# Performance work log

Measured on AMD Instinct MI355X. Metric: run time of the kernel, lower is better.

## Reference

```python
import jax, jax.numpy as jnp
import numpy as np

B, S, H, NH, NL, G, D, A, T = 32, 512, 512, 8, 6, 8, 256, 18, 1024
HD = H // NH


def setup_inputs() -> dict:
    key = jax.random.key(0)
    ks = jax.random.split(key, 32)
    def n(k, shape, s=0.02):
        return jax.random.normal(k, shape, jnp.float32) * s
    return {
        'game_indices': jax.random.randint(ks[0], (B,), 0, G),
        'states': jax.random.normal(ks[1], (B, S, D), jnp.float32),
        'actions': jax.random.randint(ks[2], (B, S), 0, A),
        'returns_to_go': jax.random.normal(ks[3], (B, S), jnp.float32),
        'timesteps': jax.random.randint(ks[4], (B, S), 0, T),
        'attention_mask': jnp.ones((B, S), jnp.int32),
        'game_emb': n(ks[5], (G, H)),
        'obs_W': n(ks[6], (G, D, H)),
        'obs_b': n(ks[7], (G, H)),
        'obs_ln_g': jnp.ones((G, H), jnp.float32),
        'obs_ln_b': jnp.zeros((G, H), jnp.float32),
        'act_emb': n(ks[8], (G, A, H)),
        'ret_W': n(ks[9], (H,)),
        'ret_b': n(ks[10], (H,)),
        'time_emb': n(ks[11], (T, H)),
        'Wqkv': n(ks[12], (NL, 3 * H, H)),
        'bqkv': n(ks[13], (NL, 3 * H)),
        'Wo': n(ks[14], (NL, H, H)),
        'bo': n(ks[15], (NL, H)),
        'ln1_g': jnp.ones((NL, H), jnp.float32),
        'ln1_b': jnp.zeros((NL, H), jnp.float32),
        'W1': n(ks[16], (NL, 4 * H, H)),
        'b1': n(ks[17], (NL, 4 * H)),
        'W2': n(ks[18], (NL, H, 4 * H)),
        'b2': n(ks[19], (NL, H)),
        'ln2_g': jnp.ones((NL, H), jnp.float32),
        'ln2_b': jnp.zeros((NL, H), jnp.float32),
        'sh_W': n(ks[20], (G, H, D)),
        'sh_b': n(ks[21], (G, D)),
        'ah_W': n(ks[22], (G, H, A)),
        'ah_b': n(ks[23], (G, A)),
        'rh_W': n(ks[24], (H, 1)),
        'rh_b': n(ks[25], (1,)),
    }


def _ln(x, g, b, eps=1e-5):
    m = jnp.mean(x, -1, keepdims=True)
    v = jnp.mean((x - m) ** 2, -1, keepdims=True)
    return (x - m) / jnp.sqrt(v + eps) * g + b


def reference(game_indices, states, actions, returns_to_go, timesteps, attention_mask,
              game_emb, obs_W, obs_b, obs_ln_g, obs_ln_b, act_emb, ret_W, ret_b, time_emb,
              Wqkv, bqkv, Wo, bo, ln1_g, ln1_b, W1, b1, W2, b2, ln2_g, ln2_b,
              sh_W, sh_b, ah_W, ah_b, rh_W, rh_b):
    gi = game_indices
    g_emb = game_emb[gi][:, None, :]  # [B,1,H]
    # per-game routed observation embedding: Linear -> LayerNorm -> ReLU (grouped GEMM by game)
    se = jnp.einsum('bsd,bdh->bsh', states, obs_W[gi]) + obs_b[gi][:, None, :]
    se = jax.nn.relu(_ln(se, obs_ln_g[gi][:, None, :], obs_ln_b[gi][:, None, :]))
    # per-game routed action embedding table lookup
    ae = act_emb[gi[:, None], actions]  # [B,S,H]
    re = returns_to_go[..., None] * ret_W + ret_b  # Linear(1,H)
    te = time_emb[timesteps]
    x = se + ae + re + te + g_emb
    # key padding mask (src_key_padding_mask: True where attention_mask==0)
    bias = jnp.where((attention_mask == 0)[:, None, None, :], -1e9, 0.0)  # [B,1,1,S]
    scale = 1.0 / jnp.sqrt(jnp.asarray(HD, jnp.float32))
    for l in range(NL):  # post-norm TransformerEncoderLayer, relu, dropout=0 (eval)
        qkv = jnp.einsum('bsh,oh->bso', x, Wqkv[l]) + bqkv[l]
        q, k, v = jnp.split(qkv, 3, axis=-1)
        q = q.reshape(B, S, NH, HD).transpose(0, 2, 1, 3)
        k = k.reshape(B, S, NH, HD).transpose(0, 2, 1, 3)
        v = v.reshape(B, S, NH, HD).transpose(0, 2, 1, 3)
        scores = jnp.einsum('bhqd,bhkd->bhqk', q, k) * scale + bias
        attn = jnp.einsum('bhqk,bhkd->bhqd', jax.nn.softmax(scores, -1), v)
        attn = attn.transpose(0, 2, 1, 3).reshape(B, S, H)
        attn = jnp.einsum('bsh,oh->bso', attn, Wo[l]) + bo[l]
        x = _ln(x + attn, ln1_g[l], ln1_b[l])
        ff = jax.nn.relu(jnp.einsum('bsh,fh->bsf', x, W1[l]) + b1[l])
        ff = jnp.einsum('bsf,hf->bsh', ff, W2[l]) + b2[l]
        x = _ln(x + ff, ln2_g[l], ln2_b[l])
    # per-game routed prediction heads
    state_preds = jnp.einsum('bsh,bho->bso', x, sh_W[gi]) + sh_b[gi][:, None, :]
    action_preds = jnp.einsum('bsh,bho->bso', x, ah_W[gi]) + ah_b[gi][:, None, :]
    return_preds = x @ rh_W + rh_b
    return (state_preds, action_preds, return_preds)
```

## Files before the change

kernel.cpp:

```cpp
#include <hip/hip_runtime.h>

typedef __bf16 bf16x4 __attribute__((ext_vector_type(4)));
typedef __bf16 bf16x8 __attribute__((ext_vector_type(8)));
typedef float f32x4 __attribute__((ext_vector_type(4)));
typedef int int4v __attribute__((ext_vector_type(4)));

#define C1SM  0.18033688011112042592f

typedef const __attribute__((address_space(1))) void gvoid_t;
typedef __attribute__((address_space(3))) void lvoid_t;


__global__ void cvt_f32_bf16(const float* __restrict__ src, __bf16* __restrict__ dst, int n4)
{
    int i = blockIdx.x * blockDim.x + threadIdx.x;
    if (i >= n4) return;
    f32x4 v = *reinterpret_cast<const f32x4*>(src + (size_t)i * 4);
    bf16x4 o;
    #pragma unroll
    for (int k = 0; k < 4; ++k) o[k] = (__bf16)v[k];
    *reinterpret_cast<bf16x4*>(dst + (size_t)i * 4) = o;
}

__global__ void transpose_cvt(const float* __restrict__ src, __bf16* __restrict__ dst, int R, int C)
{
    int m = blockIdx.y;
    int n = R * C;
    int i = blockIdx.x * 256 + threadIdx.x;
    if (i >= n) return;
    int c = i / R, r = i - c * R;
    dst[(size_t)m * n + i] = (__bf16)src[(size_t)m * n + (size_t)r * C + c];
}

__global__ void transpose_f32(const float* __restrict__ src, float* __restrict__ dst, int R, int C)
{
    int m = blockIdx.y;
    int n = R * C;
    int i = blockIdx.x * 256 + threadIdx.x;
    if (i >= n) return;
    int c = i / R, r = i - c * R;
    dst[(size_t)m * n + i] = src[(size_t)m * n + (size_t)r * C + c];
}

__global__ __launch_bounds__(256, 4)
void gemm_bt(const __bf16* __restrict__ A, size_t strideA,
             const __bf16* __restrict__ B, size_t strideB,
             const float* __restrict__ bias, int strideBias,
             float* Cf, __bf16* Cb, size_t strideC,
             const int* __restrict__ gidx,
             int K, int ldc, int relu, __bf16* __restrict__ vt)
{
    __shared__ __align__(16) char smem[32768];
    __bf16* lCb = (__bf16*)smem;
    float*  lCf = (float*)smem;

    const int z = blockIdx.z;
    const int g = gidx ? gidx[z] : 0;
    const __bf16* Ab = A + (size_t)z * strideA;
    const __bf16* Bb = B + (size_t)g * strideB;

    const int nx = gridDim.x;
    const int nwg = nx * gridDim.y;
    int orig = blockIdx.y * nx + blockIdx.x;
    int wg = ((nwg & 7) == 0) ? ((orig & 7) * (nwg >> 3) + (orig >> 3)) : orig;
    const int bm = (wg / nx) * 128, bn = (wg % nx) * 128;

    const int t = threadIdx.x;
    const int w = t >> 6, lane = t & 63;
    const int wr = (w >> 1) * 64, wc = (w & 1) * 64;
    const int l16 = lane & 15, lk = lane >> 4;

    const int srow = lane >> 2;
    const int schunk = (lane & 3) ^ (srow & 3);
    const int ca = (lk ^ (l16 & 3)) * 8;

    f32x4 acc[4][4] = {};

    auto stage = [&](int buf, int kt) {
        __bf16* la = (__bf16*)(smem + buf * 16384);
        __bf16* lb = la + 4096;
        #pragma unroll
        for (int jj = 0; jj < 2; ++jj) {
            const __bf16* ga = Ab + (size_t)(bm + w * 32 + jj * 16 + srow) * K + kt + schunk * 8;
            __builtin_amdgcn_global_load_lds((gvoid_t*)ga, (lvoid_t*)&la[(w * 32 + jj * 16) * 32], 16, 0, 0);
            const __bf16* gb = Bb + (size_t)(bn + w * 32 + jj * 16 + srow) * K + kt + schunk * 8;
            __builtin_amdgcn_global_load_lds((gvoid_t*)gb, (lvoid_t*)&lb[(w * 32 + jj * 16) * 32], 16, 0, 0);
        }
    };

    stage(0, 0);
    __syncthreads();
    int cur = 0;
    for (int kt = 0; kt < K; kt += 32) {
        if (kt + 32 < K) stage(cur ^ 1, kt + 32);
        __bf16* la = (__bf16*)(smem + cur * 16384);
        __bf16* lb = la + 4096;
        bf16x8 af[4], bfr[4];
        #pragma unroll
        for (int i = 0; i < 4; ++i) {
            af[i]  = *reinterpret_cast<const bf16x8*>(&la[(wr + i * 16 + l16) * 32 + ca]);
            bfr[i] = *reinterpret_cast<const bf16x8*>(&lb[(wc + i * 16 + l16) * 32 + ca]);
        }
        #pragma unroll
        for (int mi = 0; mi < 4; ++mi)
            #pragma unroll
            for (int ni = 0; ni < 4; ++ni)
                acc[mi][ni] = __builtin_amdgcn_mfma_f32_16x16x32_bf16(af[mi], bfr[ni], acc[mi][ni], 0, 0, 0);
        __syncthreads();
        cur ^= 1;
    }

    const float* biasb = bias ? bias + (size_t)g * strideBias : nullptr;

    if (vt && bn >= 1024) {
        const int bb = bm >> 9;
        const int s0 = (bm & 511) + wr + lk * 4;
        #pragma unroll
        for (int ni = 0; ni < 4; ++ni) {
            int c = bn + wc + ni * 16 + l16;
            float bv = biasb ? biasb[c] : 0.f;
            int hh = (c - 1024) >> 6, d = c & 63;
            __bf16* vrow = vt + ((size_t)(bb * 8 + hh) * 64 + d) * 512;
            #pragma unroll
            for (int mi = 0; mi < 4; ++mi) {
                bf16x4 o;
                #pragma unroll
                for (int j = 0; j < 4; ++j) o[j] = (__bf16)(acc[mi][ni][j] + bv);
                *reinterpret_cast<bf16x4*>(vrow + s0 + mi * 16) = o;
            }
        }
        return;
    }

    if (Cb) {
        #pragma unroll
        for (int ni = 0; ni < 4; ++ni) {
            int col = wc + ni * 16 + l16;
            float bv = biasb ? biasb[bn + col] : 0.f;
            #pragma unroll
            for (int mi = 0; mi < 4; ++mi)
                #pragma unroll
                for (int j = 0; j < 4; ++j) {
                    float v = acc[mi][ni][j] + bv;
                    if (relu) v = fmaxf(v, 0.f);
                    lCb[(wr + mi * 16 + lk * 4 + j) * 128 + col] = (__bf16)v;
                }
        }
        __syncthreads();
        #pragma unroll
        for (int it = 0; it < 8; ++it) {
            int off = it * 2048 + t * 8;
            int rl = off >> 7, col = off & 127;
            *reinterpret_cast<int4v*>(Cb + (size_t)z * strideC + (size_t)(bm + rl) * ldc + bn + col) =
                *reinterpret_cast<const int4v*>(&lCb[off]);
        }
    } else {
        #pragma unroll
        for (int p = 0; p < 2; ++p) {
            if (p) __syncthreads();
            if (wr == p * 64) {
                #pragma unroll
                for (int ni = 0; ni < 4; ++ni) {
                    int col = wc + ni * 16 + l16;
                    float bv = biasb ? biasb[bn + col] : 0.f;
                    #pragma unroll
                    for (int mi = 0; mi < 4; ++mi)
                        #pragma unroll
                        for (int j = 0; j < 4; ++j) {
                            float v = acc[mi][ni][j] + bv;
                            if (relu) v = fmaxf(v, 0.f);
                            lCf[(mi * 16 + lk * 4 + j) * 128 + col] = v;
                        }
                }
            }
            __syncthreads();
            #pragma unroll
            for (int it = 0; it < 8; ++it) {
                int off = it * 1024 + t * 4;
                int rl = off >> 7, col = off & 127;
                *reinterpret_cast<f32x4*>(Cf + (size_t)z * strideC + (size_t)(bm + p * 64 + rl) * ldc + bn + col) =
                    *reinterpret_cast<const f32x4*>(&lCf[off]);
            }
        }
    }
}

__global__ __launch_bounds__(256, 6)
void attn_fwd(const __bf16* __restrict__ qkv, const __bf16* __restrict__ vt,
              const int* __restrict__ mask, __bf16* __restrict__ out)
{
    __shared__ __bf16 lK[2][64 * 64];
    __shared__ __bf16 lP[4][16 * 32];
    __shared__ float lM2[512];

    const int bh = blockIdx.x;
    const int b = bh >> 3, h = bh & 7;
    const int q0 = blockIdx.y * 64;
    const int t = threadIdx.x, w = t >> 6, lane = t & 63;
    const int l16 = lane & 15, lk = lane >> 4;

    const __bf16* qbase = qkv + (size_t)b * 512 * 1536 + h * 64;
    const __bf16* kbase = qbase + 512;
    const __bf16* vtb = vt + (size_t)(b * 8 + h) * 64 * 512;

    bf16x8 qfr[2];
    {
        int row = q0 + w * 16 + l16;
        #pragma unroll
        for (int kc = 0; kc < 2; ++kc)
            qfr[kc] = *reinterpret_cast<const bf16x8*>(qbase + (size_t)row * 1536 + (kc * 4 + lk) * 8);
    }

    {
        int i0 = t * 2;
        lM2[i0]     = (mask[b * 512 + i0] == 0)     ? -2e9f : 0.f;
        lM2[i0 + 1] = (mask[b * 512 + i0 + 1] == 0) ? -2e9f : 0.f;
    }

    auto stageK = [&](int buf, int kt) {
        #pragma unroll
        for (int r = 0; r < 2; ++r) {
            int c = r * 256 + w * 64 + lane;
            int row = c >> 3, ch = c & 7;
            const __bf16* ga = kbase + (size_t)(kt + row) * 1536 + ((ch ^ (row & 7)) * 8);
            __builtin_amdgcn_global_load_lds((gvoid_t*)ga,
                (lvoid_t*)(&lK[buf][0] + (r * 256 + w * 64) * 8), 16, 0, 0);
        }
    };

    float m_run = -1e30f, l_run = 0.f;
    f32x4 oacc[4] = {};
    const int xsw = ((l16 >> 1) & 3) << 1;

    stageK(0, 0);
    __syncthreads();

    int cur = 0;
    for (int kt = 0; kt < 512; kt += 64) {
        if (kt + 64 < 512) stageK(cur ^ 1, kt + 64);
        const __bf16* lKc = &lK[cur][0];

        f32x4 sacc[4] = {};
        #pragma unroll
        for (int ni = 0; ni < 4; ++ni) {
            int krow = ni * 16 + l16;
            #pragma unroll
            for (int kc = 0; kc < 2; ++kc) {
                bf16x8 kf = *reinterpret_cast<const bf16x8*>(&lKc[krow * 64 + (((kc * 4 + lk) ^ (krow & 7)) * 8)]);
                sacc[ni] = __builtin_amdgcn_mfma_f32_16x16x32_bf16(kf, qfr[kc], sacc[ni], 0, 0, 0);
            }
        }

        f32x4 mx4 = {-3e38f, -3e38f, -3e38f, -3e38f};
        #pragma unroll
        for (int ni = 0; ni < 4; ++ni) {
            f32x4 mkv = *reinterpret_cast<const f32x4*>(&lM2[kt + ni * 16 + lk * 4]);
            f32x4 sv;
            #pragma unroll
            for (int j = 0; j < 4; ++j) {
                sv[j] = fmaf(sacc[ni][j], C1SM, mkv[j]);
                mx4[j] = fmaxf(mx4[j], sv[j]);
            }
            sacc[ni] = sv;
        }
        float mx = fmaxf(fmaxf(mx4[0], mx4[1]), fmaxf(mx4[2], mx4[3]));
        mx = fmaxf(mx, __shfl_xor(mx, 16));
        mx = fmaxf(mx, __shfl_xor(mx, 32));
        bool need = mx > m_run + 11.54f;
        if (__any((int)need)) {
            float mn = fmaxf(m_run, mx);
            float alpha = exp2f(m_run - mn);
            m_run = mn;
            l_run *= alpha;
            #pragma unroll
            for (int j = 0; j < 4; ++j) {
                float aj = __shfl(alpha, lk * 4 + j);
                #pragma unroll
                for (int dn = 0; dn < 4; ++dn) oacc[dn][j] *= aj;
            }
        }
        f32x4 ps4 = {0.f, 0.f, 0.f, 0.f};
        #pragma unroll
        for (int ni = 0; ni < 4; ++ni)
            #pragma unroll
            for (int j = 0; j < 4; ++j) {
                float p = exp2f(sacc[ni][j] - m_run);
                sacc[ni][j] = p;
                ps4[j] += p;
            }
        l_run += (ps4[0] + ps4[1]) + (ps4[2] + ps4[3]);

        __bf16* lp = &lP[w][0];
        #pragma unroll
        for (int kc = 0; kc < 2; ++kc) {
            #pragma unroll
            for (int n2 = 0; n2 < 2; ++n2) {
                bf16x4 o;
                #pragma unroll
                for (int j = 0; j < 4; ++j) o[j] = (__bf16)sacc[kc * 2 + n2][j];
                *reinterpret_cast<bf16x4*>(&lp[l16 * 32 + ((n2 * 4 + lk) ^ xsw) * 4]) = o;
            }
            bf16x8 pf = *reinterpret_cast<const bf16x8*>(&lp[l16 * 32 + (lk ^ (xsw >> 1)) * 8]);
            #pragma unroll
            for (int dn = 0; dn < 4; ++dn) {
                bf16x8 vf = *reinterpret_cast<const bf16x8*>(vtb + (size_t)(dn * 16 + l16) * 512 + kt + kc * 32 + lk * 8);
                oacc[dn] = __builtin_amdgcn_mfma_f32_16x16x32_bf16(pf, vf, oacc[dn], 0, 0, 0);
            }
        }
        __syncthreads();
        cur ^= 1;
    }

    float s = l_run;
    s += __shfl_xor(s, 16);
    s += __shfl_xor(s, 32);
    float linv = 1.f / s;
    #pragma unroll
    for (int j = 0; j < 4; ++j) {
        float lj = __shfl(linv, lk * 4 + j);
        #pragma unroll
        for (int dn = 0; dn < 4; ++dn) {
            int row = q0 + w * 16 + lk * 4 + j;
            int col = h * 64 + dn * 16 + l16;
            out[(size_t)(b * 512 + row) * 512 + col] = (__bf16)(oacc[dn][j] * lj);
        }
    }
}


__device__ __forceinline__ float wsum64(float v)
{
    #pragma unroll
    for (int d = 32; d >= 1; d >>= 1) v += __shfl_xor(v, d);
    return v;
}

__global__ __launch_bounds__(256)
void ln_fuse(const float* resid, const __bf16* __restrict__ proj,
             const float* __restrict__ gamma, const float* __restrict__ beta,
             float* xfo, __bf16* __restrict__ xbo)
{
    int tok = blockIdx.x * 4 + (threadIdx.x >> 6);
    int lane = threadIdx.x & 63;
    size_t base = (size_t)tok * 512 + lane * 8;
    float y[8];
    {
        f32x4 a0 = *reinterpret_cast<const f32x4*>(resid + base);
        f32x4 a1 = *reinterpret_cast<const f32x4*>(resid + base + 4);
        bf16x8 pv = *reinterpret_cast<const bf16x8*>(proj + base);
        #pragma unroll
        for (int i = 0; i < 4; ++i) { y[i] = a0[i] + (float)pv[i]; y[4 + i] = a1[i] + (float)pv[4 + i]; }
    }
    float s = 0.f;
    #pragma unroll
    for (int i = 0; i < 8; ++i) s += y[i];
    float mean = wsum64(s) * (1.f / 512.f);
    float v = 0.f;
    #pragma unroll
    for (int i = 0; i < 8; ++i) { float d = y[i] - mean; v += d * d; }
    float rstd = rsqrtf(wsum64(v) * (1.f / 512.f) + 1e-5f);
    int hh = lane * 8;
    f32x4 g0 = *reinterpret_cast<const f32x4*>(gamma + hh);
    f32x4 g1 = *reinterpret_cast<const f32x4*>(gamma + hh + 4);
    f32x4 b0 = *reinterpret_cast<const f32x4*>(beta + hh);
    f32x4 b1 = *reinterpret_cast<const f32x4*>(beta + hh + 4);
    f32x4 o0, o1;
    bf16x8 ob;
    #pragma unroll
    for (int i = 0; i < 4; ++i) {
        float t0 = (y[i] - mean) * rstd * g0[i] + b0[i];
        float t1 = (y[4 + i] - mean) * rstd * g1[i] + b1[i];
        o0[i] = t0; o1[i] = t1;
        ob[i] = (__bf16)t0; ob[4 + i] = (__bf16)t1;
    }
    *reinterpret_cast<f32x4*>(xfo + base) = o0;
    *reinterpret_cast<f32x4*>(xfo + base + 4) = o1;
    *reinterpret_cast<bf16x8*>(xbo + base) = ob;
}

__global__ __launch_bounds__(256)
void embed_fin(const __bf16* __restrict__ seraw, const int* __restrict__ gi,
               const int* __restrict__ actions, const float* __restrict__ rtg,
               const int* __restrict__ ts,
               const float* __restrict__ olg, const float* __restrict__ olb,
               const float* __restrict__ act_emb, const float* __restrict__ retW,
               const float* __restrict__ retb, const float* __restrict__ time_emb,
               const float* __restrict__ game_emb,
               float* __restrict__ xfo, __bf16* __restrict__ xbo)
{
    int tok = blockIdx.x * 4 + (threadIdx.x >> 6);
    int lane = threadIdx.x & 63;
    int b = tok >> 9;
    int g = gi[b];
    int a = actions[tok];
    int tt = ts[tok];
    float rv = rtg[tok];
    size_t base = (size_t)tok * 512 + lane * 8;
    int hh = lane * 8;

    float y[8];
    {
        bf16x8 a0 = *reinterpret_cast<const bf16x8*>(seraw + base);
        #pragma unroll
        for (int i = 0; i < 8; ++i) y[i] = (float)a0[i];
    }
    float s = 0.f;
    #pragma unroll
    for (int i = 0; i < 8; ++i) s += y[i];
    float mean = wsum64(s) * (1.f / 512.f);
    float v = 0.f;
    #pragma unroll
    for (int i = 0; i < 8; ++i) { float d = y[i] - mean; v += d * d; }
    float rstd = rsqrtf(wsum64(v) * (1.f / 512.f) + 1e-5f);

    const float* gp = olg + (size_t)g * 512 + hh;
    const float* bp = olb + (size_t)g * 512 + hh;
    const float* ap = act_emb + ((size_t)g * 18 + a) * 512 + hh;
    const float* tp = time_emb + (size_t)tt * 512 + hh;
    const float* ep = game_emb + (size_t)g * 512 + hh;
    const float* rwp = retW + hh;
    const float* rbp = retb + hh;

    f32x4 o0, o1;
    bf16x8 ob;
    #pragma unroll
    for (int half = 0; half < 2; ++half) {
        f32x4 gv = *reinterpret_cast<const f32x4*>(gp + half * 4);
        f32x4 bv = *reinterpret_cast<const f32x4*>(bp + half * 4);
        f32x4 av = *reinterpret_cast<const f32x4*>(ap + half * 4);
        f32x4 tv = *reinterpret_cast<const f32x4*>(tp + half * 4);
        f32x4 ev = *reinterpret_cast<const f32x4*>(ep + half * 4);
        f32x4 rw = *reinterpret_cast<const f32x4*>(rwp + half * 4);
        f32x4 rb = *reinterpret_cast<const f32x4*>(rbp + half * 4);
        #pragma unroll
        for (int i = 0; i < 4; ++i) {
            float n = (y[half * 4 + i] - mean) * rstd * gv[i] + bv[i];
            n = fmaxf(n, 0.f);
            float o = n + av[i] + rv * rw[i] + rb[i] + tv[i] + ev[i];
            if (half == 0) o0[i] = o; else o1[i] = o;
            ob[half * 4 + i] = (__bf16)o;
        }
    }
    *reinterpret_cast<f32x4*>(xfo + base) = o0;
    *reinterpret_cast<f32x4*>(xfo + base + 4) = o1;
    *reinterpret_cast<bf16x8*>(xbo + base) = ob;
}

__global__ __launch_bounds__(256)
void head_ar(const float* __restrict__ xf, const int* __restrict__ gi,
             const float* __restrict__ ahWt, const float* __restrict__ ah_b,
             const float* __restrict__ rhW, const float* __restrict__ rhb,
             float* __restrict__ outA, float* __restrict__ outR)
{
    int tok = blockIdx.x * 4 + (threadIdx.x >> 6);
    int lane = threadIdx.x & 63;
    int b = tok >> 9;
    int g = gi[b];
    size_t base = (size_t)tok * 512 + lane * 8;
    float x[8];
    {
        f32x4 a0 = *reinterpret_cast<const f32x4*>(xf + base);
        f32x4 a1 = *reinterpret_cast<const f32x4*>(xf + base + 4);
        #pragma unroll
        for (int i = 0; i < 4; ++i) { x[i] = a0[i]; x[4 + i] = a1[i]; }
    }
    #pragma unroll 1
    for (int a = 0; a < 18; ++a) {
        const float* wp = ahWt + ((size_t)g * 18 + a) * 512 + lane * 8;
        f32x4 w0 = *reinterpret_cast<const f32x4*>(wp);
        f32x4 w1 = *reinterpret_cast<const f32x4*>(wp + 4);
        float p = 0.f;
        #pragma unroll
        for (int i = 0; i < 4; ++i) { p += x[i] * w0[i]; p += x[4 + i] * w1[i]; }
        p = wsum64(p);
        if (lane == 0) outA[(size_t)tok * 18 + a] = p + ah_b[g * 18 + a];
    }
    {
        const float* wp = rhW + lane * 8;
        f32x4 w0 = *reinterpret_cast<const f32x4*>(wp);
        f32x4 w1 = *reinterpret_cast<const f32x4*>(wp + 4);
        float p = 0.f;
        #pragma unroll
        for (int i = 0; i < 4; ++i) { p += x[i] * w0[i]; p += x[4 + i] * w1[i]; }
        p = wsum64(p);
        if (lane == 0) outR[tok] = p + rhb[0];
    }
}


extern "C" void kernel_launch(void* const* d_in, const int* in_sizes, int n_in,
                              void* d_out, int out_size, void* d_ws, size_t ws_size,
                              hipStream_t stream)
{
    (void)in_sizes; (void)n_in; (void)out_size; (void)ws_size;

    const int*   gi       = (const int*)d_in[0];
    const float* states   = (const float*)d_in[1];
    const int*   actions  = (const int*)d_in[2];
    const float* rtg      = (const float*)d_in[3];
    const int*   ts       = (const int*)d_in[4];
    const int*   amask    = (const int*)d_in[5];
    const float* game_emb = (const float*)d_in[6];
    const float* obs_W    = (const float*)d_in[7];
    const float* obs_b    = (const float*)d_in[8];
    const float* obs_ln_g = (const float*)d_in[9];
    const float* obs_ln_b = (const float*)d_in[10];
    const float* act_emb  = (const float*)d_in[11];
    const float* ret_W    = (const float*)d_in[12];
    const float* ret_b    = (const float*)d_in[13];
    const float* time_emb = (const float*)d_in[14];
    const float* Wqkv     = (const float*)d_in[15];
    const float* bqkv     = (const float*)d_in[16];
    const float* Wo       = (const float*)d_in[17];
    const float* bo       = (const float*)d_in[18];
    const float* ln1_g    = (const float*)d_in[19];
    const float* ln1_b    = (const float*)d_in[20];
    const float* W1       = (const float*)d_in[21];
    const float* b1       = (const float*)d_in[22];
    const float* W2       = (const float*)d_in[23];
    const float* b2       = (const float*)d_in[24];
    const float* ln2_g    = (const float*)d_in[25];
    const float* ln2_b    = (const float*)d_in[26];
    const float* sh_W     = (const float*)d_in[27];
    const float* sh_b     = (const float*)d_in[28];
    const float* ah_W     = (const float*)d_in[29];
    const float* ah_b     = (const float*)d_in[30];
    const float* rh_W     = (const float*)d_in[31];
    const float* rh_b     = (const float*)d_in[32];

    char* wsb = (char*)d_ws;
    float*  xf      = (float*)(wsb + 0);
    __bf16* xb      = (__bf16*)(wsb + 33554432);
    __bf16* tmp     = (__bf16*)(wsb + 50331648);
    __bf16* vT      = (__bf16*)(wsb + 67108864);
    __bf16* qkvB    = (__bf16*)(wsb + 83886080);
    __bf16* ff1B    = qkvB;
    __bf16* statesB = qkvB;
    __bf16* obswB   = (__bf16*)(wsb + 83886080 + 8388608);
    __bf16* attnB   = (__bf16*)(wsb + 150994944);
    __bf16* wqkvB   = (__bf16*)(wsb + 167772160);
    __bf16* woB     = (__bf16*)(wsb + 177209344);
    __bf16* w1B     = (__bf16*)(wsb + 180355072);
    __bf16* w2B     = (__bf16*)(wsb + 192937984);
    __bf16* shwB    = (__bf16*)(wsb + 205520896);
    float*  ahwT    = (float*)(wsb + 207618048);

    cvt_f32_bf16<<<4608, 256, 0, stream>>>(Wqkv, wqkvB, 1179648);
    cvt_f32_bf16<<<1536, 256, 0, stream>>>(Wo, woB, 393216);
    cvt_f32_bf16<<<6144, 256, 0, stream>>>(W1, w1B, 1572864);
    cvt_f32_bf16<<<6144, 256, 0, stream>>>(W2, w2B, 1572864);
    cvt_f32_bf16<<<4096, 256, 0, stream>>>(states, statesB, 1048576);
    transpose_cvt<<<dim3(512, 8), 256, 0, stream>>>(obs_W, obswB, 256, 512);
    transpose_cvt<<<dim3(512, 8), 256, 0, stream>>>(sh_W, shwB, 512, 256);
    transpose_f32<<<dim3(36, 8), 256, 0, stream>>>(ah_W, ahwT, 512, 18);

    gemm_bt<<<dim3(4, 4, 32), 256, 0, stream>>>(
        statesB, (size_t)512 * 256, obswB, (size_t)512 * 256, obs_b, 512,
        nullptr, tmp, (size_t)512 * 512, gi, 256, 512, 0, nullptr);
    embed_fin<<<4096, 256, 0, stream>>>(tmp, gi, actions, rtg, ts,
        obs_ln_g, obs_ln_b, act_emb, ret_W, ret_b, time_emb, game_emb, xf, xb);

    for (int l = 0; l < 6; ++l) {
        gemm_bt<<<dim3(12, 128, 1), 256, 0, stream>>>(
            xb, 0, wqkvB + (size_t)l * 1536 * 512, 0, bqkv + l * 1536, 0,
            nullptr, qkvB, 0, nullptr, 512, 1536, 0, vT);
        attn_fwd<<<dim3(256, 8, 1), 256, 0, stream>>>(qkvB, vT, amask, attnB);
        gemm_bt<<<dim3(4, 128, 1), 256, 0, stream>>>(
            attnB, 0, woB + (size_t)l * 512 * 512, 0, bo + l * 512, 0,
            nullptr, tmp, 0, nullptr, 512, 512, 0, nullptr);
        ln_fuse<<<4096, 256, 0, stream>>>(xf, tmp, ln1_g + l * 512, ln1_b + l * 512, xf, xb);
        gemm_bt<<<dim3(16, 128, 1), 256, 0, stream>>>(
            xb, 0, w1B + (size_t)l * 2048 * 512, 0, b1 + l * 2048, 0,
            nullptr, ff1B, 0, nullptr, 512, 2048, 1, nullptr);
        gemm_bt<<<dim3(4, 128, 1), 256, 0, stream>>>(
            ff1B, 0, w2B + (size_t)l * 512 * 2048, 0, b2 + l * 512, 0,
            nullptr, tmp, 0, nullptr, 2048, 512, 0, nullptr);
        ln_fuse<<<4096, 256, 0, stream>>>(xf, tmp, ln2_g + l * 512, ln2_b + l * 512, xf, xb);
    }

    gemm_bt<<<dim3(2, 4, 32), 256, 0, stream>>>(
        xb, (size_t)512 * 512, shwB, (size_t)256 * 512, sh_b, 256,
        (float*)d_out, nullptr, (size_t)512 * 256, gi, 512, 256, 0, nullptr);
    head_ar<<<4096, 256, 0, stream>>>(xf, gi, ahwT, ah_b, rh_W, rh_b,
        (float*)d_out + 4194304, (float*)d_out + 4489216);
}
```

Measured before the change: 1.666 ms.

## Split-K output GEMMs, 128-row attention tiles with LDS V, drop fp32 residual

```diff
diff --git a/kernel.cpp b/kernel.cpp
--- a/kernel.cpp
+++ b/kernel.cpp
@@ -47,8 +47,8 @@
              const __bf16* __restrict__ B, size_t strideB,
              const float* __restrict__ bias, int strideBias,
              float* Cf, __bf16* Cb, size_t strideC,
-             const int* __restrict__ gidx,
-             int K, int ldc, int relu, __bf16* __restrict__ vt)
+             const int* __restrict__ gidx, int ldk, int Klen,
+             size_t splitStride, int ldc, int relu, __bf16* __restrict__ vt)
 {
     __shared__ __align__(16) char smem[32768];
     __bf16* lCb = (__bf16*)smem;
@@ -56,8 +56,11 @@
 
     const int z = blockIdx.z;
     const int g = gidx ? gidx[z] : 0;
-    const __bf16* Ab = A + (size_t)z * strideA;
-    const __bf16* Bb = B + (size_t)g * strideB;
+    const __bf16* Ab = A + (splitStride ? (size_t)z * Klen : (size_t)z * strideA);
+    const __bf16* Bb = B + (splitStride ? (size_t)z * Klen : (size_t)g * strideB);
+    __bf16* CbO = Cb ? (Cb + (size_t)z * (splitStride ? splitStride : strideC)) : nullptr;
+    float*  CfO = Cf ? (Cf + (size_t)z * strideC) : nullptr;
+    const float* biasb = (bias && (!splitStride || z == 0)) ? bias + (size_t)g * strideBias : nullptr;
 
     const int nx = gridDim.x;
     const int nwg = nx * gridDim.y;
@@ -81,9 +84,9 @@
         __bf16* lb = la + 4096;
         #pragma unroll
         for (int jj = 0; jj < 2; ++jj) {
-            const __bf16* ga = Ab + (size_t)(bm + w * 32 + jj * 16 + srow) * K + kt + schunk * 8;
+            const __bf16* ga = Ab + (size_t)(bm + w * 32 + jj * 16 + srow) * ldk + kt + schunk * 8;
             __builtin_amdgcn_global_load_lds((gvoid_t*)ga, (lvoid_t*)&la[(w * 32 + jj * 16) * 32], 16, 0, 0);
-            const __bf16* gb = Bb + (size_t)(bn + w * 32 + jj * 16 + srow) * K + kt + schunk * 8;
+            const __bf16* gb = Bb + (size_t)(bn + w * 32 + jj * 16 + srow) * ldk + kt + schunk * 8;
             __builtin_amdgcn_global_load_lds((gvoid_t*)gb, (lvoid_t*)&lb[(w * 32 + jj * 16) * 32], 16, 0, 0);
         }
     };
@@ -91,8 +94,8 @@
     stage(0, 0);
     __syncthreads();
     int cur = 0;
-    for (int kt = 0; kt < K; kt += 32) {
-        if (kt + 32 < K) stage(cur ^ 1, kt + 32);
+    for (int kt = 0; kt < Klen; kt += 32) {
+        if (kt + 32 < Klen) stage(cur ^ 1, kt + 32);
         __bf16* la = (__bf16*)(smem + cur * 16384);
         __bf16* lb = la + 4096;
         bf16x8 af[4], bfr[4];
@@ -109,8 +112,6 @@
         __syncthreads();
         cur ^= 1;
     }
-
-    const float* biasb = bias ? bias + (size_t)g * strideBias : nullptr;
 
     if (vt && bn >= 1024) {
         const int bb = bm >> 9;
@@ -132,7 +133,7 @@
         return;
     }
 
-    if (Cb) {
+    if (CbO) {
         #pragma unroll
         for (int ni = 0; ni < 4; ++ni) {
             int col = wc + ni * 16 + l16;
@@ -151,7 +152,7 @@
         for (int it = 0; it < 8; ++it) {
             int off = it * 2048 + t * 8;
             int rl = off >> 7, col = off & 127;
-            *reinterpret_cast<int4v*>(Cb + (size_t)z * strideC + (size_t)(bm + rl) * ldc + bn + col) =
+            *reinterpret_cast<int4v*>(CbO + (size_t)(bm + rl) * ldc + bn + col) =
                 *reinterpret_cast<const int4v*>(&lCb[off]);
         }
     } else {
@@ -178,24 +179,25 @@
             for (int it = 0; it < 8; ++it) {
                 int off = it * 1024 + t * 4;
                 int rl = off >> 7, col = off & 127;
-                *reinterpret_cast<f32x4*>(Cf + (size_t)z * strideC + (size_t)(bm + p * 64 + rl) * ldc + bn + col) =
+                *reinterpret_cast<f32x4*>(CfO + (size_t)(bm + p * 64 + rl) * ldc + bn + col) =
                     *reinterpret_cast<const f32x4*>(&lCf[off]);
             }
         }
     }
 }
 
-__global__ __launch_bounds__(256, 6)
-void attn_fwd(const __bf16* __restrict__ qkv, const __bf16* __restrict__ vt,
-              const int* __restrict__ mask, __bf16* __restrict__ out)
+__global__ __launch_bounds__(256, 4)
+void attn_fwd_c(const __bf16* __restrict__ qkv, const __bf16* __restrict__ vt,
+                const int* __restrict__ mask, __bf16* __restrict__ out)
 {
     __shared__ __bf16 lK[2][64 * 64];
+    __shared__ __bf16 lV[2][64 * 64];
     __shared__ __bf16 lP[4][16 * 32];
     __shared__ float lM2[512];
 
     const int bh = blockIdx.x;
     const int b = bh >> 3, h = bh & 7;
-    const int q0 = blockIdx.y * 64;
+    const int q0 = blockIdx.y * 128;
     const int t = threadIdx.x, w = t >> 6, lane = t & 63;
     const int l16 = lane & 15, lk = lane >> 4;
 
@@ -203,21 +205,21 @@
     const __bf16* kbase = qbase + 512;
     const __bf16* vtb = vt + (size_t)(b * 8 + h) * 64 * 512;
 
-    bf16x8 qfr[2];
-    {
-        int row = q0 + w * 16 + l16;
+    bf16x8 qfr[2][2];
+    #pragma unroll
+    for (int qn = 0; qn < 2; ++qn) {
+        int row = q0 + w * 32 + qn * 16 + l16;
         #pragma unroll
         for (int kc = 0; kc < 2; ++kc)
-            qfr[kc] = *reinterpret_cast<const bf16x8*>(qbase + (size_t)row * 1536 + (kc * 4 + lk) * 8);
-    }
-
+            qfr[qn][kc] = *reinterpret_cast<const bf16x8*>(qbase + (size_t)row * 1536 + (kc * 4 + lk) * 8);
+    }
     {
         int i0 = t * 2;
         lM2[i0]     = (mask[b * 512 + i0] == 0)     ? -2e9f : 0.f;
         lM2[i0 + 1] = (mask[b * 512 + i0 + 1] == 0) ? -2e9f : 0.f;
     }
 
-    auto stageK = [&](int buf, int kt) {
+    auto stageKV = [&](int buf, int kt) {
         #pragma unroll
         for (int r = 0; r < 2; ++r) {
             int c = r * 256 + w * 64 + lane;
@@ -225,104 +227,115 @@
             const __bf16* ga = kbase + (size_t)(kt + row) * 1536 + ((ch ^ (row & 7)) * 8);
             __builtin_amdgcn_global_load_lds((gvoid_t*)ga,
                 (lvoid_t*)(&lK[buf][0] + (r * 256 + w * 64) * 8), 16, 0, 0);
+            const __bf16* gv = vtb + (size_t)row * 512 + kt + ((ch ^ (row & 7)) * 8);
+            __builtin_amdgcn_global_load_lds((gvoid_t*)gv,
+                (lvoid_t*)(&lV[buf][0] + (r * 256 + w * 64) * 8), 16, 0, 0);
         }
     };
 
-    float m_run = -1e30f, l_run = 0.f;
-    f32x4 oacc[4] = {};
+    float m_run[2] = {-1e30f, -1e30f}, l_run[2] = {0.f, 0.f};
+    f32x4 oacc[2][4] = {};
     const int xsw = ((l16 >> 1) & 3) << 1;
 
-    stageK(0, 0);
+    stageKV(0, 0);
     __syncthreads();
 
     int cur = 0;
     for (int kt = 0; kt < 512; kt += 64) {
-        if (kt + 64 < 512) stageK(cur ^ 1, kt + 64);
+        if (kt + 64 < 512) stageKV(cur ^ 1, kt + 64);
         const __bf16* lKc = &lK[cur][0];
-
-        f32x4 sacc[4] = {};
-        #pragma unroll
-        for (int ni = 0; ni < 4; ++ni) {
-            int krow = ni * 16 + l16;
+        const __bf16* lVc = &lV[cur][0];
+        __bf16* lp = &lP[w][0];
+
+        #pragma unroll
+        for (int qn = 0; qn < 2; ++qn) {
+            f32x4 sacc[4] = {};
+            #pragma unroll
+            for (int ni = 0; ni < 4; ++ni) {
+                int krow = ni * 16 + l16;
+                #pragma unroll
+                for (int kc = 0; kc < 2; ++kc) {
+                    bf16x8 kf = *reinterpret_cast<const bf16x8*>(&lKc[krow * 64 + (((kc * 4 + lk) ^ (krow & 7)) * 8)]);
+                    sacc[ni] = __builtin_amdgcn_mfma_f32_16x16x32_bf16(kf, qfr[qn][kc], sacc[ni], 0, 0, 0);
+                }
+            }
+
+            f32x4 mx4 = {-3e38f, -3e38f, -3e38f, -3e38f};
+            #pragma unroll
+            for (int ni = 0; ni < 4; ++ni) {
+                f32x4 mkv = *reinterpret_cast<const f32x4*>(&lM2[kt + ni * 16 + lk * 4]);
+                f32x4 sv;
+                #pragma unroll
+                for (int j = 0; j < 4; ++j) {
+                    sv[j] = fmaf(sacc[ni][j], C1SM, mkv[j]);
+                    mx4[j] = fmaxf(mx4[j], sv[j]);
+                }
+                sacc[ni] = sv;
+            }
+            float mx = fmaxf(fmaxf(mx4[0], mx4[1]), fmaxf(mx4[2], mx4[3]));
+            mx = fmaxf(mx, __shfl_xor(mx, 16));
+            mx = fmaxf(mx, __shfl_xor(mx, 32));
+            bool need = mx > m_run[qn] + 11.54f;
+            if (__any((int)need)) {
+                float mn = fmaxf(m_run[qn], mx);
+                float alpha = exp2f(m_run[qn] - mn);
+                m_run[qn] = mn;
+                l_run[qn] *= alpha;
+                #pragma unroll
+                for (int j = 0; j < 4; ++j) {
+                    float aj = __shfl(alpha, lk * 4 + j);
+                    #pragma unroll
+                    for (int dn = 0; dn < 4; ++dn) oacc[qn][dn][j] *= aj;
+                }
+            }
+            f32x4 ps4 = {0.f, 0.f, 0.f, 0.f};
+            #pragma unroll
+            for (int ni = 0; ni < 4; ++ni)
+                #pragma unroll
+                for (int j = 0; j < 4; ++j) {
+                    float p = exp2f(sacc[ni][j] - m_run[qn]);
+                    sacc[ni][j] = p;
+                    ps4[j] += p;
+                }
+            l_run[qn] += (ps4[0] + ps4[1]) + (ps4[2] + ps4[3]);
+
             #pragma unroll
             for (int kc = 0; kc < 2; ++kc) {
-                bf16x8 kf = *reinterpret_cast<const bf16x8*>(&lKc[krow * 64 + (((kc * 4 + lk) ^ (krow & 7)) * 8)]);
-                sacc[ni] = __builtin_amdgcn_mfma_f32_16x16x32_bf16(kf, qfr[kc], sacc[ni], 0, 0, 0);
-            }
-        }
-
-        f32x4 mx4 = {-3e38f, -3e38f, -3e38f, -3e38f};
-        #pragma unroll
-        for (int ni = 0; ni < 4; ++ni) {
-            f32x4 mkv = *reinterpret_cast<const f32x4*>(&lM2[kt + ni * 16 + lk * 4]);
-            f32x4 sv;
-            #pragma unroll
-            for (int j = 0; j < 4; ++j) {
-                sv[j] = fmaf(sacc[ni][j], C1SM, mkv[j]);
-                mx4[j] = fmaxf(mx4[j], sv[j]);
-            }
-            sacc[ni] = sv;
-        }
-        float mx = fmaxf(fmaxf(mx4[0], mx4[1]), fmaxf(mx4[2], mx4[3]));
-        mx = fmaxf(mx, __shfl_xor(mx, 16));
-        mx = fmaxf(mx, __shfl_xor(mx, 32));
-        bool need = mx > m_run + 11.54f;
-        if (__any((int)need)) {
-            float mn = fmaxf(m_run, mx);
-            float alpha = exp2f(m_run - mn);
-            m_run = mn;
-            l_run *= alpha;
-            #pragma unroll
-            for (int j = 0; j < 4; ++j) {
-                float aj = __shfl(alpha, lk * 4 + j);
-                #pragma unroll
-                for (int dn = 0; dn < 4; ++dn) oacc[dn][j] *= aj;
-            }
-        }
-        f32x4 ps4 = {0.f, 0.f, 0.f, 0.f};
-        #pragma unroll
-        for (int ni = 0; ni < 4; ++ni)
-            #pragma unroll
-            for (int j = 0; j < 4; ++j) {
-                float p = exp2f(sacc[ni][j] - m_run);
-                sacc[ni][j] = p;
-                ps4[j] += p;
-            }
-        l_run += (ps4[0] + ps4[1]) + (ps4[2] + ps4[3]);
-
-        __bf16* lp = &lP[w][0];
-        #pragma unroll
-        for (int kc = 0; kc < 2; ++kc) {
-            #pragma unroll
-            for (int n2 = 0; n2 < 2; ++n2) {
-                bf16x4 o;
-                #pragma unroll
-                for (int j = 0; j < 4; ++j) o[j] = (__bf16)sacc[kc * 2 + n2][j];
-                *reinterpret_cast<bf16x4*>(&lp[l16 * 32 + ((n2 * 4 + lk) ^ xsw) * 4]) = o;
-            }
-            bf16x8 pf = *reinterpret_cast<const bf16x8*>(&lp[l16 * 32 + (lk ^ (xsw >> 1)) * 8]);
-            #pragma unroll
-            for (int dn = 0; dn < 4; ++dn) {
-                bf16x8 vf = *reinterpret_cast<const bf16x8*>(vtb + (size_t)(dn * 16 + l16) * 512 + kt + kc * 32 + lk * 8);
-                oacc[dn] = __builtin_amdgcn_mfma_f32_16x16x32_bf16(pf, vf, oacc[dn], 0, 0, 0);
+                #pragma unroll
+                for (int n2 = 0; n2 < 2; ++n2) {
+                    bf16x4 o;
+                    #pragma unroll
+                    for (int j = 0; j < 4; ++j) o[j] = (__bf16)sacc[kc * 2 + n2][j];
+                    *reinterpret_cast<bf16x4*>(&lp[l16 * 32 + ((n2 * 4 + lk) ^ xsw) * 4]) = o;
+                }
+                bf16x8 pf = *reinterpret_cast<const bf16x8*>(&lp[l16 * 32 + (lk ^ (xsw >> 1)) * 8]);
+                #pragma unroll
+                for (int dn = 0; dn < 4; ++dn) {
+                    int vrow = dn * 16 + l16;
+                    bf16x8 vf = *reinterpret_cast<const bf16x8*>(&lVc[vrow * 64 + (((kc * 4 + lk) ^ (vrow & 7)) * 8)]);
+                    oacc[qn][dn] = __builtin_amdgcn_mfma_f32_16x16x32_bf16(pf, vf, oacc[qn][dn], 0, 0, 0);
+                }
             }
         }
         __syncthreads();
         cur ^= 1;
     }
 
-    float s = l_run;
-    s += __shfl_xor(s, 16);
-    s += __shfl_xor(s, 32);
-    float linv = 1.f / s;
-    #pragma unroll
-    for (int j = 0; j < 4; ++j) {
-        float lj = __shfl(linv, lk * 4 + j);
-        #pragma unroll
-        for (int dn = 0; dn < 4; ++dn) {
-            int row = q0 + w * 16 + lk * 4 + j;
-            int col = h * 64 + dn * 16 + l16;
-            out[(size_t)(b * 512 + row) * 512 + col] = (__bf16)(oacc[dn][j] * lj);
+    #pragma unroll
+    for (int qn = 0; qn < 2; ++qn) {
+        float s = l_run[qn];
+        s += __shfl_xor(s, 16);
+        s += __shfl_xor(s, 32);
+        float linv = 1.f / s;
+        #pragma unroll
+        for (int j = 0; j < 4; ++j) {
+            float lj = __shfl(linv, lk * 4 + j);
+            #pragma unroll
+            for (int dn = 0; dn < 4; ++dn) {
+                int row = q0 + w * 32 + qn * 16 + lk * 4 + j;
+                int col = h * 64 + dn * 16 + l16;
+                out[(size_t)(b * 512 + row) * 512 + col] = (__bf16)(oacc[qn][dn][j] * lj);
+            }
         }
     }
 }
@@ -336,20 +349,21 @@
 }
 
 __global__ __launch_bounds__(256)
-void ln_fuse(const float* resid, const __bf16* __restrict__ proj,
-             const float* __restrict__ gamma, const float* __restrict__ beta,
-             float* xfo, __bf16* __restrict__ xbo)
+void ln_fuse2(const __bf16* resid, const __bf16* __restrict__ pA,
+              const __bf16* __restrict__ pB,
+              const float* __restrict__ gamma, const float* __restrict__ beta,
+              __bf16* xbo)
 {
     int tok = blockIdx.x * 4 + (threadIdx.x >> 6);
     int lane = threadIdx.x & 63;
     size_t base = (size_t)tok * 512 + lane * 8;
     float y[8];
     {
-        f32x4 a0 = *reinterpret_cast<const f32x4*>(resid + base);
-        f32x4 a1 = *reinterpret_cast<const f32x4*>(resid + base + 4);
-        bf16x8 pv = *reinterpret_cast<const bf16x8*>(proj + base);
-        #pragma unroll
-        for (int i = 0; i < 4; ++i) { y[i] = a0[i] + (float)pv[i]; y[4 + i] = a1[i] + (float)pv[4 + i]; }
+        bf16x8 rv = *reinterpret_cast<const bf16x8*>(resid + base);
+        bf16x8 pa = *reinterpret_cast<const bf16x8*>(pA + base);
+        bf16x8 pb = *reinterpret_cast<const bf16x8*>(pB + base);
+        #pragma unroll
+        for (int i = 0; i < 8; ++i) y[i] = (float)rv[i] + (float)pa[i] + (float)pb[i];
     }
     float s = 0.f;
     #pragma unroll
@@ -364,17 +378,12 @@
     f32x4 g1 = *reinterpret_cast<const f32x4*>(gamma + hh + 4);
     f32x4 b0 = *reinterpret_cast<const f32x4*>(beta + hh);
     f32x4 b1 = *reinterpret_cast<const f32x4*>(beta + hh + 4);
-    f32x4 o0, o1;
     bf16x8 ob;
     #pragma unroll
     for (int i = 0; i < 4; ++i) {
-        float t0 = (y[i] - mean) * rstd * g0[i] + b0[i];
-        float t1 = (y[4 + i] - mean) * rstd * g1[i] + b1[i];
-        o0[i] = t0; o1[i] = t1;
-        ob[i] = (__bf16)t0; ob[4 + i] = (__bf16)t1;
-    }
-    *reinterpret_cast<f32x4*>(xfo + base) = o0;
-    *reinterpret_cast<f32x4*>(xfo + base + 4) = o1;
+        ob[i]     = (__bf16)((y[i] - mean) * rstd * g0[i] + b0[i]);
+        ob[4 + i] = (__bf16)((y[4 + i] - mean) * rstd * g1[i] + b1[i]);
+    }
     *reinterpret_cast<bf16x8*>(xbo + base) = ob;
 }
 
@@ -386,7 +395,7 @@
                const float* __restrict__ act_emb, const float* __restrict__ retW,
                const float* __restrict__ retb, const float* __restrict__ time_emb,
                const float* __restrict__ game_emb,
-               float* __restrict__ xfo, __bf16* __restrict__ xbo)
+               __bf16* __restrict__ xbo)
 {
     int tok = blockIdx.x * 4 + (threadIdx.x >> 6);
     int lane = threadIdx.x & 63;
@@ -421,7 +430,6 @@
     const float* rwp = retW + hh;
     const float* rbp = retb + hh;
 
-    f32x4 o0, o1;
     bf16x8 ob;
     #pragma unroll
     for (int half = 0; half < 2; ++half) {
@@ -437,17 +445,14 @@
             float n = (y[half * 4 + i] - mean) * rstd * gv[i] + bv[i];
             n = fmaxf(n, 0.f);
             float o = n + av[i] + rv * rw[i] + rb[i] + tv[i] + ev[i];
-            if (half == 0) o0[i] = o; else o1[i] = o;
             ob[half * 4 + i] = (__bf16)o;
         }
     }
-    *reinterpret_cast<f32x4*>(xfo + base) = o0;
-    *reinterpret_cast<f32x4*>(xfo + base + 4) = o1;
     *reinterpret_cast<bf16x8*>(xbo + base) = ob;
 }
 
 __global__ __launch_bounds__(256)
-void head_ar(const float* __restrict__ xf, const int* __restrict__ gi,
+void head_ar(const __bf16* __restrict__ xbv, const int* __restrict__ gi,
              const float* __restrict__ ahWt, const float* __restrict__ ah_b,
              const float* __restrict__ rhW, const float* __restrict__ rhb,
              float* __restrict__ outA, float* __restrict__ outR)
@@ -459,10 +464,9 @@
     size_t base = (size_t)tok * 512 + lane * 8;
     float x[8];
     {
-        f32x4 a0 = *reinterpret_cast<const f32x4*>(xf + base);
-        f32x4 a1 = *reinterpret_cast<const f32x4*>(xf + base + 4);
-        #pragma unroll
-        for (int i = 0; i < 4; ++i) { x[i] = a0[i]; x[4 + i] = a1[i]; }
+        bf16x8 a0 = *reinterpret_cast<const bf16x8*>(xbv + base);
+        #pragma unroll
+        for (int i = 0; i < 8; ++i) x[i] = (float)a0[i];
     }
     #pragma unroll 1
     for (int a = 0; a < 18; ++a) {
@@ -529,9 +533,9 @@
     const float* rh_b     = (const float*)d_in[32];
 
     char* wsb = (char*)d_ws;
-    float*  xf      = (float*)(wsb + 0);
+    __bf16* tmp     = (__bf16*)(wsb + 0);
+    __bf16* tmp2    = tmp + 8388608;
     __bf16* xb      = (__bf16*)(wsb + 33554432);
-    __bf16* tmp     = (__bf16*)(wsb + 50331648);
     __bf16* vT      = (__bf16*)(wsb + 67108864);
     __bf16* qkvB    = (__bf16*)(wsb + 83886080);
     __bf16* ff1B    = qkvB;
@@ -556,31 +560,31 @@
 
     gemm_bt<<<dim3(4, 4, 32), 256, 0, stream>>>(
         statesB, (size_t)512 * 256, obswB, (size_t)512 * 256, obs_b, 512,
-        nullptr, tmp, (size_t)512 * 512, gi, 256, 512, 0, nullptr);
+        nullptr, tmp, (size_t)512 * 512, gi, 256, 256, 0, 512, 0, nullptr);
     embed_fin<<<4096, 256, 0, stream>>>(tmp, gi, actions, rtg, ts,
-        obs_ln_g, obs_ln_b, act_emb, ret_W, ret_b, time_emb, game_emb, xf, xb);
+        obs_ln_g, obs_ln_b, act_emb, ret_W, ret_b, time_emb, game_emb, xb);
 
     for (int l = 0; l < 6; ++l) {
         gemm_bt<<<dim3(12, 128, 1), 256, 0, stream>>>(
             xb, 0, wqkvB + (size_t)l * 1536 * 512, 0, bqkv + l * 1536, 0,
-            nullptr, qkvB, 0, nullptr, 512, 1536, 0, vT);
-        attn_fwd<<<dim3(256, 8, 1), 256, 0, stream>>>(qkvB, vT, amask, attnB);
-        gemm_bt<<<dim3(4, 128, 1), 256, 0, stream>>>(
+            nullptr, qkvB, 0, nullptr, 512, 512, 0, 1536, 0, vT);
+        attn_fwd_c<<<dim3(256, 4, 1), 256, 0, stream>>>(qkvB, vT, amask, attnB);
+        gemm_bt<<<dim3(4, 128, 2), 256, 0, stream>>>(
             attnB, 0, woB + (size_t)l * 512 * 512, 0, bo + l * 512, 0,
-            nullptr, tmp, 0, nullptr, 512, 512, 0, nullptr);
-        ln_fuse<<<4096, 256, 0, stream>>>(xf, tmp, ln1_g + l * 512, ln1_b + l * 512, xf, xb);
+            nullptr, tmp, 0, nullptr, 512, 256, 8388608, 512, 0, nullptr);
+        ln_fuse2<<<4096, 256, 0, stream>>>(xb, tmp, tmp2, ln1_g + l * 512, ln1_b + l * 512, xb);
         gemm_bt<<<dim3(16, 128, 1), 256, 0, stream>>>(
             xb, 0, w1B + (size_t)l * 2048 * 512, 0, b1 + l * 2048, 0,
-            nullptr, ff1B, 0, nullptr, 512, 2048, 1, nullptr);
-        gemm_bt<<<dim3(4, 128, 1), 256, 0, stream>>>(
+            nullptr, ff1B, 0, nullptr, 512, 512, 0, 2048, 1, nullptr);
+        gemm_bt<<<dim3(4, 128, 2), 256, 0, stream>>>(
             ff1B, 0, w2B + (size_t)l * 512 * 2048, 0, b2 + l * 512, 0,
-            nullptr, tmp, 0, nullptr, 2048, 512, 0, nullptr);
-        ln_fuse<<<4096, 256, 0, stream>>>(xf, tmp, ln2_g + l * 512, ln2_b + l * 512, xf, xb);
+            nullptr, tmp, 0, nullptr, 2048, 1024, 8388608, 512, 0, nullptr);
+        ln_fuse2<<<4096, 256, 0, stream>>>(xb, tmp, tmp2, ln2_g + l * 512, ln2_b + l * 512, xb);
     }
 
     gemm_bt<<<dim3(2, 4, 32), 256, 0, stream>>>(
         xb, (size_t)512 * 512, shwB, (size_t)256 * 512, sh_b, 256,
-        (float*)d_out, nullptr, (size_t)512 * 256, gi, 512, 256, 0, nullptr);
-    head_ar<<<4096, 256, 0, stream>>>(xf, gi, ahwT, ah_b, rh_W, rh_b,
+        (float*)d_out, nullptr, (size_t)512 * 256, gi, 512, 512, 0, 256, 0, nullptr);
+    head_ar<<<4096, 256, 0, stream>>>(xb, gi, ahwT, ah_b, rh_W, rh_b,
         (float*)d_out + 4194304, (float*)d_out + 4489216);
 }
```

Result: faster. 1.408 ms (-15.5%).
